# Kernel tuning notes

Measured on AMD Instinct MI355X. Metric: run time of the kernel, lower is better.

The kernel has to match this reference:

```python
import jax, jax.numpy as jnp
import numpy as np

F_NUM, F_DIM, O_DIM, K = 16, 32, 2, 16
B, T, C = 256, 48, 3000
V = K + 2  # code vocabulary: 0 unused, 1 = missing, 2..K+1 = centroid ids
NEG_BIG = 1e7


def setup_inputs() -> dict:
    key = jax.random.key(0)
    ks = jax.random.split(key, 16)
    return {
        "tdata": jax.random.normal(ks[0], (B, T, F_NUM, F_DIM), jnp.float32),
        "f_mask": jax.random.randint(ks[1], (B, T, F_NUM), 0, 2) > 0,
        "centers": jax.random.normal(ks[2], (F_NUM, K, F_DIM), jnp.float32),
        "pat": jax.random.randint(ks[3], (F_NUM, C, F_NUM), 0, V),
        "pat_rep": jax.random.normal(ks[4], (F_NUM, C, F_DIM), jnp.float32),
        "pos_cnt": jax.random.uniform(ks[5], (F_NUM, C), jnp.float32),
        "neg_cnt": jax.random.uniform(ks[6], (F_NUM, C), jnp.float32),
        "W_q": jax.random.normal(ks[7], (F_NUM, F_DIM, F_DIM), jnp.float32) * 0.1,
        "b_q": jax.random.normal(ks[8], (F_NUM, F_DIM), jnp.float32) * 0.1,
        "W_k": jax.random.normal(ks[9], (F_NUM, F_DIM, F_DIM + 1), jnp.float32) * 0.1,
        "b_k": jax.random.normal(ks[10], (F_NUM, F_DIM), jnp.float32) * 0.1,
        "W_v": jax.random.normal(ks[11], (F_NUM, F_DIM + 1, F_DIM + 1), jnp.float32) * 0.1,
        "b_v": jax.random.normal(ks[12], (F_NUM, F_DIM + 1), jnp.float32) * 0.1,
        "W_pred": jax.random.normal(ks[13], (O_DIM, F_NUM * (F_DIM + 1)), jnp.float32) * 0.1,
    }


def _forward(tdata, f_mask, centers, pat, pat_rep, pos_cnt, neg_cnt,
             W_q, b_q, W_k, b_k, W_v, b_v, W_pred):
    Bs, Ts, Fn, D = tdata.shape
    N = Bs * Ts
    fdata = tdata.reshape(N, Fn, D)

    # --- compute_codes: nearest-centroid assignment per feature (vectorized) ---
    # dist[n,i,k] = ||fdata[n,i]||^2 - 2 <fdata[n,i], centers[i,k]> + ||centers[i,k]||^2
    d_norm = jnp.sum(fdata * fdata, axis=-1, keepdims=True)            # [N,F,1]
    c_norm = jnp.sum(centers * centers, axis=-1)                        # [F,K]
    dots = jnp.einsum('nid,ikd->nik', fdata, centers)                   # [N,F,K]
    dists = d_norm - 2.0 * dots + c_norm[None]                          # [N,F,K]
    pos_codes = jnp.argmin(dists, axis=-1) + 2                          # [N,F]
    maskNF = f_mask.reshape(N, Fn)
    f_codes = jnp.where(maskNF, pos_codes, 1)                           # [N,F] int, 1 = missing

    # one-hot codes, shared across feature loop: [N, F, V]
    oh = jax.nn.one_hot(f_codes, V, dtype=jnp.float32)

    q_last = tdata[:, -1]                                               # [B,F,D]
    reps, atts = [], []
    for i in range(Fn):
        pat_i = pat[i]                                                  # [C,F]
        # A[c,j,v]=1 iff pattern slot is wildcard (0) or code v matches pat
        eq = jnp.arange(V)[None, None, :] == pat_i[:, :, None]
        A = jnp.where((pat_i == 0)[:, :, None], True, eq).astype(jnp.float32)
        # count of matching slots; match iff all F slots match
        cnt = jnp.einsum('njv,cjv->nc', oh, A)                          # [N,C]
        match_nc = cnt >= (Fn - 0.5)
        pm = jnp.any(match_nc.reshape(Bs, Ts, C), axis=1)               # [B,C] any over time
        pm_f = pm.astype(jnp.float32)

        pos_ratio = pos_cnt[i] / (pos_cnt[i] + neg_cnt[i] + 1e-6)       # [C]
        rep_aug = jnp.concatenate([pat_rep[i], pos_ratio[:, None]], 1)  # [C,D+1]
        key_i = pm_f[:, :, None] * rep_aug[None]                        # [B,C,D+1]

        # FinalAttentionQKV, attention_type='mul'
        iq = q_last[:, i] @ W_q[i].T + b_q[i]                           # [B,D]
        ik = key_i @ W_k[i].T + b_k[i]                                  # [B,C,D]
        iv = key_i @ W_v[i].T + b_v[i]                                  # [B,C,D+1]
        e = jnp.einsum('bcd,bd->bc', ik, iq)
        e = e - (1.0 - pm_f) * NEG_BIG
        a = jax.nn.softmax(e, axis=-1)
        v = jnp.einsum('bc,bce->be', a, iv)                             # [B,D+1]
        reps.append(v)
        atts.append(a)

    rep = jnp.stack(reps, axis=1)                                       # [B,F,D+1]
    rep = rep * jnp.any(f_mask, axis=1)[:, :, None].astype(rep.dtype)
    cohort_cali = rep.reshape(Bs, -1) @ W_pred.T                        # [B,o_dim]
    cohort_a = jnp.stack(atts, axis=0)                                  # [F,B,C]
    return cohort_cali, cohort_a, rep


def reference(tdata, f_mask, centers, pat, pat_rep, pos_cnt, neg_cnt,
              W_q, b_q, W_k, b_k, W_v, b_v, W_pred):
    return _forward(tdata, f_mask, centers, pat, pat_rep, pos_cnt, neg_cnt,
                    W_q, b_q, W_k, b_k, W_v, b_v, W_pred)
```

## Files before the change

kernel.cpp:

```cpp
#include <hip/hip_runtime.h>
#include <stdint.h>

#define FN 16
#define FD 32
#define KC 16
#define BS 256
#define TS 48
#define CS 3000
#define VV 18
#define NW 96
#define NEG_BIG 10000000.0f

__global__ __launch_bounds__(256) void k_codes(const float* __restrict__ tdata,
                                               const int* __restrict__ f_mask,
                                               const float* __restrict__ centers,
                                               uint8_t* __restrict__ codes) {
    __shared__ float cnorm_s[256];
    int tid = threadIdx.x;
    {
        const float* c = centers + (size_t)tid * FD;
        float cn = 0.f;
#pragma unroll
        for (int d = 0; d < FD; d++) { float cv = c[d]; cn += cv * cv; }
        cnorm_s[tid] = cn;
    }
    __syncthreads();

    int idx = blockIdx.x * 256 + tid;
    int j = idx & 15;
    const float* x = tdata + (size_t)idx * FD;
    float xv[FD];
#pragma unroll
    for (int d = 0; d < FD; d++) xv[d] = x[d];
    const float* cen = centers + (size_t)j * KC * FD;
    float best = 3.4e38f; int bestk = 0;
    for (int k = 0; k < KC; k++) {
        float dot = 0.f;
#pragma unroll
        for (int d = 0; d < FD; d++) dot += xv[d] * cen[k * FD + d];
        float dist = cnorm_s[(j << 4) + k] - 2.f * dot;
        if (dist < best) { best = dist; bestk = k; }
    }
    codes[idx] = f_mask[idx] ? (uint8_t)(bestk + 2) : (uint8_t)1;
}

__global__ __launch_bounds__(64) void k_buildM(const int* __restrict__ pat,
                                               uint32_t* __restrict__ M) {
    int idx = blockIdx.x * 64 + threadIdx.x;
    if (idx >= FN * FN * NW) return;
    int cg = idx % NW;
    int ij = idx / NW;
    int j = ij & 15, i = ij >> 4;
    int c0 = cg * 32;
    int p[32];
#pragma unroll
    for (int cb = 0; cb < 32; cb++) {
        int c = c0 + cb;
        p[cb] = (c < CS) ? pat[((size_t)i * CS + c) * FN + j] : -1;
    }
    uint32_t w0 = 0u;
#pragma unroll
    for (int cb = 0; cb < 32; cb++) w0 |= (p[cb] == 0) ? (1u << cb) : 0u;
    uint32_t* dst = M + (size_t)ij * VV * NW + cg;
#pragma unroll
    for (int v = 0; v < VV; v++) {
        uint32_t w = w0;
#pragma unroll
        for (int cb = 0; cb < 32; cb++) w |= (p[cb] == v) ? (1u << cb) : 0u;
        dst[(size_t)v * NW] = w;
    }
}

__global__ void k_match(const uint8_t* __restrict__ codes, const uint32_t* __restrict__ M,
                        uint32_t* __restrict__ pm) {
    int b = blockIdx.x & 255;
    int i = blockIdx.x >> 8;
    int cg = threadIdx.x;
    __shared__ uint8_t cs[TS * FN];
    for (int k = threadIdx.x; k < TS * FN; k += blockDim.x)
        cs[k] = codes[(size_t)b * TS * FN + k];
    __syncthreads();
    const uint32_t* Mi = M + (size_t)i * FN * VV * NW;
    uint32_t acc = 0;
    for (int t = 0; t < TS; t++) {
        uint32_t m = 0xFFFFFFFFu;
#pragma unroll
        for (int jj = 0; jj < FN; jj++) {
            int v = cs[t * FN + jj];
            m &= Mi[((size_t)jj * VV + v) * NW + cg];
            if (!m) break;
        }
        acc |= m;
    }
    pm[(size_t)blockIdx.x * NW + cg] = acc;
}

__global__ __launch_bounds__(256) void k_attn(
    const float* __restrict__ tdata, const float* __restrict__ pat_rep,
    const float* __restrict__ pos_cnt, const float* __restrict__ neg_cnt,
    const float* __restrict__ W_q, const float* __restrict__ b_q,
    const float* __restrict__ W_k, const float* __restrict__ b_k,
    const float* __restrict__ W_v, const float* __restrict__ b_v,
    const uint32_t* __restrict__ pm, const int* __restrict__ f_mask,
    float* __restrict__ out_a, float* __restrict__ out_rep)
{
    int b = blockIdx.x & 255;
    int i = blockIdx.x >> 8;
    int tid = threadIdx.x;

    __shared__ float e_s[CS];
    __shared__ float iq_s[FD];
    __shared__ float kq_s[FD + 1];
    __shared__ float s_sh[FD + 1];
    __shared__ float red[4];
    __shared__ float bkiq_s, maxv_s, sum_s;
    __shared__ int any_s;

    int mbit = (tid < TS) ? f_mask[((size_t)b * TS + tid) * FN + i] : 0;
    unsigned long long bal = __ballot(mbit != 0);
    if (tid == 0) any_s = (bal != 0ULL);

    const float* q = tdata + (((size_t)b * TS + (TS - 1)) * FN + i) * FD;
    if (tid >= 64 && tid < 64 + FD) {
        int r = tid - 64;
        float acc = b_q[i * FD + r];
        const float* Wr = W_q + ((size_t)i * FD + r) * FD;
#pragma unroll
        for (int e = 0; e < FD; e++) acc += q[e] * Wr[e];
        iq_s[r] = acc;
    }
    if (tid < FD + 1) s_sh[tid] = 0.f;
    __syncthreads();
    if (tid < FD + 1) {
        float acc = 0.f;
        for (int d = 0; d < FD; d++)
            acc += W_k[((size_t)i * FD + d) * (FD + 1) + tid] * iq_s[d];
        kq_s[tid] = acc;
    }
    if (tid == 64) {
        float acc = 0.f;
        for (int d = 0; d < FD; d++) acc += b_k[i * FD + d] * iq_s[d];
        bkiq_s = acc;
    }
    __syncthreads();
    float bkiq = bkiq_s;

    const uint32_t* pmrow = pm + (size_t)blockIdx.x * NW;

    float lmax = -3.4e38f;
    for (int c = tid; c < CS; c += 256) {
        uint32_t bit = (pmrow[c >> 5] >> (c & 31)) & 1u;
        float e;
        if (bit) {
            const float* pr = pat_rep + ((size_t)i * CS + c) * FD;
            float acc = 0.f;
#pragma unroll
            for (int d = 0; d < FD; d++) acc += pr[d] * kq_s[d];
            float pc = pos_cnt[(size_t)i * CS + c], nc = neg_cnt[(size_t)i * CS + c];
            float ratio = pc / (pc + nc + 1e-6f);
            e = bkiq + acc + ratio * kq_s[FD];
        } else {
            e = bkiq - NEG_BIG;
        }
        e_s[c] = e;
        lmax = fmaxf(lmax, e);
    }
    for (int off = 32; off > 0; off >>= 1) lmax = fmaxf(lmax, __shfl_down(lmax, off));
    if ((tid & 63) == 0) red[tid >> 6] = lmax;
    __syncthreads();
    if (tid == 0) {
        float m = red[0];
        for (int w = 1; w < 4; w++) m = fmaxf(m, red[w]);
        maxv_s = m;
    }
    __syncthreads();
    float maxv = maxv_s;

    float lsum = 0.f;
    for (int c = tid; c < CS; c += 256) {
        float ex = __expf(e_s[c] - maxv);
        e_s[c] = ex;
        lsum += ex;
    }
    for (int off = 32; off > 0; off >>= 1) lsum += __shfl_down(lsum, off);
    if ((tid & 63) == 0) red[tid >> 6] = lsum;
    __syncthreads();
    if (tid == 0) sum_s = red[0] + red[1] + red[2] + red[3];
    __syncthreads();
    float sum = sum_s;

    float* arow = out_a + (size_t)blockIdx.x * CS;
    for (int c = tid; c < CS; c += 256) {
        float a = e_s[c] / sum;
        arow[c] = a;
        uint32_t bit = (pmrow[c >> 5] >> (c & 31)) & 1u;
        if (bit) {
            const float* pr = pat_rep + ((size_t)i * CS + c) * FD;
            for (int f = 0; f < FD; f++) atomicAdd(&s_sh[f], a * pr[f]);
            float pc = pos_cnt[(size_t)i * CS + c], nc = neg_cnt[(size_t)i * CS + c];
            float ratio = pc / (pc + nc + 1e-6f);
            atomicAdd(&s_sh[FD], a * ratio);
        }
    }
    __syncthreads();

    if (tid < FD + 1) {
        float acc = b_v[(size_t)i * (FD + 1) + tid];
        const float* Wr = W_v + ((size_t)i * (FD + 1) + tid) * (FD + 1);
#pragma unroll
        for (int f = 0; f < FD + 1; f++) acc += Wr[f] * s_sh[f];
        float r = any_s ? acc : 0.f;
        out_rep[((size_t)b * FN + i) * (FD + 1) + tid] = r;
    }
}

__global__ __launch_bounds__(256) void k_cali(const float* __restrict__ rep,
                                              const float* __restrict__ W_pred,
                                              float* __restrict__ out) {
    int b = blockIdx.x;
    int tid = threadIdx.x;
    const int KK = FN * (FD + 1);
    float a0 = 0.f, a1 = 0.f;
    for (int k = tid; k < KK; k += 256) {
        float r = rep[(size_t)b * KK + k];
        a0 += r * W_pred[k];
        a1 += r * W_pred[KK + k];
    }
    for (int off = 32; off > 0; off >>= 1) {
        a0 += __shfl_down(a0, off);
        a1 += __shfl_down(a1, off);
    }
    __shared__ float r0[4], r1[4];
    if ((tid & 63) == 0) { r0[tid >> 6] = a0; r1[tid >> 6] = a1; }
    __syncthreads();
    if (tid == 0) {
        out[b * 2 + 0] = r0[0] + r0[1] + r0[2] + r0[3];
        out[b * 2 + 1] = r1[0] + r1[1] + r1[2] + r1[3];
    }
}

extern "C" void kernel_launch(void* const* d_in, const int* in_sizes, int n_in,
                              void* d_out, int out_size, void* d_ws, size_t ws_size,
                              hipStream_t stream) {
    const float* tdata   = (const float*)d_in[0];
    const int*   f_mask  = (const int*)d_in[1];
    const float* centers = (const float*)d_in[2];
    const int*   pat     = (const int*)d_in[3];
    const float* pat_rep = (const float*)d_in[4];
    const float* pos_cnt = (const float*)d_in[5];
    const float* neg_cnt = (const float*)d_in[6];
    const float* W_q     = (const float*)d_in[7];
    const float* b_q     = (const float*)d_in[8];
    const float* W_k     = (const float*)d_in[9];
    const float* b_k     = (const float*)d_in[10];
    const float* W_v     = (const float*)d_in[11];
    const float* b_v     = (const float*)d_in[12];
    const float* W_pred  = (const float*)d_in[13];

    float* out = (float*)d_out;
    float* out_cali = out;
    float* out_a    = out + 512;
    float* out_rep  = out + 512 + FN * BS * CS;

    char* ws = (char*)d_ws;
    uint8_t*  codes = (uint8_t*)ws;
    uint32_t* M     = (uint32_t*)(ws + 200704);
    uint32_t* pm    = (uint32_t*)(ws + 200704 + 1769472);

    hipLaunchKernelGGL(k_codes,   dim3((BS * TS * FN) / 256), dim3(256), 0, stream,
                       tdata, f_mask, centers, codes);
    hipLaunchKernelGGL(k_buildM,  dim3((FN * FN * NW) / 64), dim3(64), 0, stream,
                       pat, M);
    hipLaunchKernelGGL(k_match,   dim3(FN * BS), dim3(NW), 0, stream,
                       codes, M, pm);
    hipLaunchKernelGGL(k_attn,    dim3(FN * BS), dim3(256), 0, stream,
                       tdata, pat_rep, pos_cnt, neg_cnt, W_q, b_q, W_k, b_k, W_v, b_v,
                       pm, f_mask, out_a, out_rep);
    hipLaunchKernelGGL(k_cali,    dim3(BS), dim3(256), 0, stream,
                       out_rep, W_pred, out_cali);
}
```

Before: 248.5 us.

## Restructure code assignment and mask building for coalesced access and wave ballots

k_codes now gives each block one feature j and 64 rows. It stages the rows through shared memory with float4 loads, so every thread in the block reads the same centroids (a broadcast). k_buildM now maps lanes to patterns and builds each 64-bit mask word with __ballot instead of each thread looping over 32 strided pattern reads. Both changes target uncoalesced global loads in the preprocessing kernels. These kernels are likely a small part of total time next to k_attn, and the new ballot loop is serialised over j and v.

```diff
diff --git a/kernel.cpp b/kernel.cpp
--- a/kernel.cpp
+++ b/kernel.cpp
@@ -11,63 +11,71 @@
 #define NW 96
 #define NEG_BIG 10000000.0f
 
-__global__ __launch_bounds__(256) void k_codes(const float* __restrict__ tdata,
-                                               const int* __restrict__ f_mask,
-                                               const float* __restrict__ centers,
-                                               uint8_t* __restrict__ codes) {
-    __shared__ float cnorm_s[256];
-    int tid = threadIdx.x;
-    {
-        const float* c = centers + (size_t)tid * FD;
+__global__ __launch_bounds__(64) void k_codes(const float* __restrict__ tdata,
+                                              const int* __restrict__ f_mask,
+                                              const float* __restrict__ centers,
+                                              uint8_t* __restrict__ codes) {
+    __shared__ float xs[64][33];
+    __shared__ float cns[KC];
+    int t   = threadIdx.x;
+    int bid = blockIdx.x;
+    int j   = bid & 15;
+    int n0  = (bid >> 4) << 6;
+
+    const float* cen = centers + (size_t)j * KC * FD;
+
+    if (t < KC) {
         float cn = 0.f;
 #pragma unroll
-        for (int d = 0; d < FD; d++) { float cv = c[d]; cn += cv * cv; }
-        cnorm_s[tid] = cn;
-    }
-    __syncthreads();
-
-    int idx = blockIdx.x * 256 + tid;
-    int j = idx & 15;
-    const float* x = tdata + (size_t)idx * FD;
+        for (int d = 0; d < FD; d++) { float cv = cen[t * FD + d]; cn += cv * cv; }
+        cns[t] = cn;
+    }
+
+#pragma unroll
+    for (int it = 0; it < 8; ++it) {
+        int f = t + (it << 6);
+        int row = f >> 3, q = f & 7;
+        float4 v = *reinterpret_cast<const float4*>(
+            tdata + ((size_t)(n0 + row) * FN + j) * FD + (q << 2));
+        xs[row][(q << 2) + 0] = v.x;
+        xs[row][(q << 2) + 1] = v.y;
+        xs[row][(q << 2) + 2] = v.z;
+        xs[row][(q << 2) + 3] = v.w;
+    }
+    __syncthreads();
+
     float xv[FD];
 #pragma unroll
-    for (int d = 0; d < FD; d++) xv[d] = x[d];
-    const float* cen = centers + (size_t)j * KC * FD;
+    for (int d = 0; d < FD; d++) xv[d] = xs[t][d];
+
     float best = 3.4e38f; int bestk = 0;
     for (int k = 0; k < KC; k++) {
         float dot = 0.f;
 #pragma unroll
         for (int d = 0; d < FD; d++) dot += xv[d] * cen[k * FD + d];
-        float dist = cnorm_s[(j << 4) + k] - 2.f * dot;
+        float dist = cns[k] - 2.f * dot;
         if (dist < best) { best = dist; bestk = k; }
     }
+    int idx = (n0 + t) * FN + j;
     codes[idx] = f_mask[idx] ? (uint8_t)(bestk + 2) : (uint8_t)1;
 }
 
 __global__ __launch_bounds__(64) void k_buildM(const int* __restrict__ pat,
                                                uint32_t* __restrict__ M) {
-    int idx = blockIdx.x * 64 + threadIdx.x;
-    if (idx >= FN * FN * NW) return;
-    int cg = idx % NW;
-    int ij = idx / NW;
-    int j = ij & 15, i = ij >> 4;
-    int c0 = cg * 32;
-    int p[32];
-#pragma unroll
-    for (int cb = 0; cb < 32; cb++) {
-        int c = c0 + cb;
-        p[cb] = (c < CS) ? pat[((size_t)i * CS + c) * FN + j] : -1;
-    }
-    uint32_t w0 = 0u;
-#pragma unroll
-    for (int cb = 0; cb < 32; cb++) w0 |= (p[cb] == 0) ? (1u << cb) : 0u;
-    uint32_t* dst = M + (size_t)ij * VV * NW + cg;
-#pragma unroll
-    for (int v = 0; v < VV; v++) {
-        uint32_t w = w0;
-#pragma unroll
-        for (int cb = 0; cb < 32; cb++) w |= (p[cb] == v) ? (1u << cb) : 0u;
-        dst[(size_t)v * NW] = w;
+    int lane = threadIdx.x;
+    int bid  = blockIdx.x;
+    int i = bid / 47, g = bid % 47;
+    int c = (g << 6) + lane;
+    bool valid = (c < CS);
+    for (int j = 0; j < FN; j++) {
+        int p = valid ? pat[((size_t)i * CS + c) * FN + j] : -1;
+        bool wild = (p == 0);
+        uint32_t* dst = M + (((size_t)((i << 4) | j) * VV) * NW) + (g << 1);
+        for (int v = 0; v < VV; v++) {
+            unsigned long long bal = __ballot(wild || (p == v));
+            if (lane < 2) dst[(size_t)v * NW + lane] =
+                (lane == 0) ? (uint32_t)bal : (uint32_t)(bal >> 32);
+        }
     }
 }
 
@@ -267,9 +275,9 @@
     uint32_t* M     = (uint32_t*)(ws + 200704);
     uint32_t* pm    = (uint32_t*)(ws + 200704 + 1769472);
 
-    hipLaunchKernelGGL(k_codes,   dim3((BS * TS * FN) / 256), dim3(256), 0, stream,
+    hipLaunchKernelGGL(k_codes,   dim3(16 * 192), dim3(64), 0, stream,
                        tdata, f_mask, centers, codes);
-    hipLaunchKernelGGL(k_buildM,  dim3((FN * FN * NW) / 64), dim3(64), 0, stream,
+    hipLaunchKernelGGL(k_buildM,  dim3(16 * 47), dim3(64), 0, stream,
                        pat, M);
     hipLaunchKernelGGL(k_match,   dim3(FN * BS), dim3(NW), 0, stream,
                        codes, M, pm);
```

Result: slower. 306.2 us (+23.2%).
